# Performance work log

Hardware: AMD Instinct MI355X
Metric: run time of the kernel (lower is better)

The kernel has to match this reference:

```python
import jax, jax.numpy as jnp
import numpy as np

N, E, T = 10000, 50000, 80000   # nodes, edges, triplets
D, H, C, CF = 16, 128, 64, 64   # n_orb, hidden_dim, conv_dim, coeffs_dim


def l2norm(v):
    # matches torch F.normalize(dim=-1): x / max(||x||_2, 1e-12)
    return v / jnp.maximum(jnp.linalg.norm(v, axis=-1, keepdims=True), 1e-12)


def setup_inputs() -> dict:
    key = jax.random.key(0)
    ks = jax.random.split(key, 16)

    def w(k, i, o):
        return jax.random.normal(k, (i, o), jnp.float32) / np.sqrt(i).astype(np.float32)

    return {
        "x": jax.random.normal(ks[0], (N, H), jnp.float32),
        "cji": jax.random.normal(ks[1], (E, D, CF), jnp.float32),
        "robs": jax.random.normal(ks[2], (E, D), jnp.float32),
        "shbs": jax.random.normal(ks[3], (T, D), jnp.float32),
        "idx_i": jax.random.randint(ks[4], (E,), 0, N),
        "idx_j": jax.random.randint(ks[5], (E,), 0, N),
        "tri_idx_k": jax.random.randint(ks[6], (T,), 0, N),
        "edge_idx_kj": jax.random.randint(ks[7], (T,), 0, E),
        "edge_idx_ji": jax.random.randint(ks[8], (T,), 0, E),
        "W_nb": w(ks[9], H, 2 * C), "b_nb": jnp.zeros((2 * C,), jnp.float32),
        "W_c1": w(ks[10], CF, C),
        "W_c2": w(ks[11], C, 2 * C),
        "W_t3": w(ks[12], C, C), "b_t3": jnp.zeros((C,), jnp.float32),
        "W_n1": w(ks[13], 2 * C, C), "b_n1": jnp.zeros((C,), jnp.float32),
        "W_n2": w(ks[14], C, C), "b_n2": jnp.zeros((C,), jnp.float32),
        "W_na": w(ks[15], C, H),
    }


def reference(x, cji, robs, shbs, idx_i, idx_j, tri_idx_k, edge_idx_kj,
              edge_idx_ji, W_nb, b_nb, W_c1, W_c2, W_t3, b_t3, W_n1, b_n1,
              W_n2, b_n2, W_na):
    silu = jax.nn.silu
    # node_before_lin + chunk
    h = x @ W_nb + b_nb                       # [N, 2C]
    xq, xk = jnp.split(h, 2, axis=-1)         # each [N, C]
    # coeffs_before_lin: act -> Dense -> act -> Dense (no biases)
    c = silu(silu(cji) @ W_c1) @ W_c2         # [E, D, 2C]
    cji2, ckj = jnp.split(c, 2, axis=-1)      # each [E, D, C]
    # triplet gathers
    ckj_g = l2norm(ckj[edge_idx_kj])          # [T, D, C]
    tbo = l2norm(jnp.einsum('td,tdh->th', shbs * robs[edge_idx_kj], ckj_g))  # [T, C]
    tbw = tbo * jax.nn.sigmoid(xk[tri_idx_k])  # [T, C]
    # scatter triplets -> edges (dim_size = robs.size(0) = E)
    agg = jax.ops.segment_sum(tbw, edge_idx_ji, num_segments=E)  # [E, C]
    tbw2 = silu(agg) @ W_t3 + b_t3            # three_lin, [E, C]
    cji3 = l2norm(cji2 * (1.0 + tbw2[:, None, :]))  # cji + cji*w, normalized
    lcao = l2norm(jnp.einsum('ed,edh->eh', robs, cji3))  # [E, C]
    # node message: node_lin on concatenated endpoint features
    m = jnp.concatenate([xq[idx_i], xq[idx_j]], axis=-1)  # [E, 2C]
    m = silu(silu(m) @ W_n1 + b_n1) @ W_n2 + b_n2          # [E, C]
    out = x + jax.ops.segment_sum(lcao * m, idx_i, num_segments=N) @ W_na
    return out
```

## Files before the change

### kernel.cpp

```cpp
#include <hip/hip_runtime.h>
#include <hip/hip_bf16.h>

#define NN 10000
#define EE 50000
#define TT 80000
#define DD 16
#define HH 128
#define CC 64

typedef __hip_bfloat16 bf16;
typedef __attribute__((ext_vector_type(8))) short bf16x8;
typedef __attribute__((ext_vector_type(4))) short bf16x4;
typedef __attribute__((ext_vector_type(4))) float f32x4;

__device__ __forceinline__ float silu_f(float x) {
  return x * __builtin_amdgcn_rcpf(1.f + __expf(-x));
}
__device__ __forceinline__ float sigm_f(float x) {
  return __builtin_amdgcn_rcpf(1.f + __expf(-x));
}

__device__ __forceinline__ short f2bs(float x) {
  __hip_bfloat16 h = __float2bfloat16(x);
  short s;
  __builtin_memcpy(&s, &h, 2);
  return s;
}

__device__ __forceinline__ float rnorm_f(float ss) {
  return __builtin_amdgcn_rcpf(fmaxf(__builtin_amdgcn_sqrtf(ss), 1e-12f));
}

__device__ __forceinline__ void bf2x(unsigned u, float& lo, float& hi) {
  lo = __uint_as_float(u << 16);
  hi = __uint_as_float(u & 0xffff0000u);
}

#define ZERO_U4 960000

__global__ __launch_bounds__(128) void k_node(
    const float* __restrict__ x, const float* __restrict__ W_nb,
    const float* __restrict__ b_nb, float* __restrict__ sxq,
    float* __restrict__ sigxk, uint4* __restrict__ zero_p) {
  __shared__ __align__(16) float xs[8][HH];
  const int t = threadIdx.x;
  const int base = blockIdx.x * 8;
#pragma unroll
  for (int i = 0; i < 8; ++i) xs[i][t] = x[(size_t)(base + i) * HH + t];
  for (int i = blockIdx.x * 128 + t; i < ZERO_U4; i += (NN / 8) * 128)
    zero_p[i] = (uint4){0u, 0u, 0u, 0u};
  __syncthreads();
  float acc[8];
  const float bb = b_nb[t];
#pragma unroll
  for (int i = 0; i < 8; ++i) acc[i] = bb;
  for (int k = 0; k < HH; k += 4) {
    const float w0 = W_nb[(k + 0) * HH + t];
    const float w1 = W_nb[(k + 1) * HH + t];
    const float w2 = W_nb[(k + 2) * HH + t];
    const float w3 = W_nb[(k + 3) * HH + t];
#pragma unroll
    for (int i = 0; i < 8; ++i) {
      const float4 xv = *(const float4*)(&xs[i][k]);
      acc[i] = fmaf(xv.x, w0, acc[i]);
      acc[i] = fmaf(xv.y, w1, acc[i]);
      acc[i] = fmaf(xv.z, w2, acc[i]);
      acc[i] = fmaf(xv.w, w3, acc[i]);
    }
  }
  if (t < CC) {
#pragma unroll
    for (int i = 0; i < 8; ++i)
      sxq[(size_t)(base + i) * CC + t] = silu_f(acc[i]);
  } else {
#pragma unroll
    for (int i = 0; i < 8; ++i)
      sigxk[(size_t)(base + i) * CC + (t - CC)] = sigm_f(acc[i]);
  }
}

#define K2_BLOCKS 2048
#define K2_TILES 50000
__global__ __launch_bounds__(256, 2) void k_coeffs(
    const float* __restrict__ cji, const float* __restrict__ W_c1,
    const float* __restrict__ W_c2, bf16* __restrict__ cji2,
    bf16* __restrict__ ckjn) {
  const int tid = threadIdx.x;
  const int w = tid >> 6, l = tid & 63;
  const int lr = l & 15, lg = l >> 4;

  bf16x4 bw1[4][4];
  bf16x4 bw2[4][8];
#pragma unroll
  for (int rt = 0; rt < 4; ++rt)
#pragma unroll
    for (int kt = 0; kt < 4; ++kt) {
      bf16x4 t;
#pragma unroll
      for (int b = 0; b < 4; ++b)
        t[b] = f2bs(W_c1[(kt * 16 + lg * 4 + b) * 64 + rt * 16 + lr]);
      bw1[rt][kt] = t;
    }
#pragma unroll
  for (int kt = 0; kt < 4; ++kt)
#pragma unroll
    for (int ct = 0; ct < 8; ++ct) {
      bf16x4 t;
#pragma unroll
      for (int b = 0; b < 4; ++b)
        t[b] = f2bs(W_c2[(kt * 16 + lg * 4 + b) * 128 + ct * 16 + lr]);
      bw2[kt][ct] = t;
    }

  const int nwave = K2_BLOCKS * 4;
  const int t0 = blockIdx.x * 4 + w;
  if (t0 >= K2_TILES) return;
  const int lane_off = lr * 64 + lg * 4;

  float4 rA[4], rB[4];
#pragma unroll
  for (int kt = 0; kt < 4; ++kt)
    rA[kt] = *(const float4*)(cji + (size_t)t0 * 1024 + lane_off + kt * 16);
  if (t0 + nwave < K2_TILES)
#pragma unroll
    for (int kt = 0; kt < 4; ++kt)
      rB[kt] = *(const float4*)(cji + (size_t)(t0 + nwave) * 1024 + lane_off + kt * 16);

  auto process = [&](int tile, float4 (&r)[4], int pref_tile) {
    bf16x4 sB[4];
#pragma unroll
    for (int kt = 0; kt < 4; ++kt) {
      bf16x4 t;
      t[0] = f2bs(silu_f(r[kt].x));
      t[1] = f2bs(silu_f(r[kt].y));
      t[2] = f2bs(silu_f(r[kt].z));
      t[3] = f2bs(silu_f(r[kt].w));
      sB[kt] = t;
    }
    if (pref_tile < K2_TILES) {
#pragma unroll
      for (int kt = 0; kt < 4; ++kt)
        r[kt] = *(const float4*)(cji + (size_t)pref_tile * 1024 + lane_off + kt * 16);
    }

    f32x4 acc1[4];
#pragma unroll
    for (int rt = 0; rt < 4; ++rt) acc1[rt] = (f32x4){0.f, 0.f, 0.f, 0.f};
#pragma unroll
    for (int rt = 0; rt < 4; ++rt)
#pragma unroll
      for (int kt = 0; kt < 4; ++kt)
        acc1[rt] = __builtin_amdgcn_mfma_f32_16x16x16bf16_1k(bw1[rt][kt], sB[kt], acc1[rt], 0, 0, 0);

    bf16x4 tf[4];
#pragma unroll
    for (int kt = 0; kt < 4; ++kt) {
      bf16x4 t;
#pragma unroll
      for (int b = 0; b < 4; ++b) t[b] = f2bs(silu_f(acc1[kt][b]));
      tf[kt] = t;
    }

    {
      f32x4 acc[4];
#pragma unroll
      for (int ct = 0; ct < 4; ++ct) acc[ct] = (f32x4){0.f, 0.f, 0.f, 0.f};
#pragma unroll
      for (int ct = 0; ct < 4; ++ct)
#pragma unroll
        for (int kt = 0; kt < 4; ++kt)
          acc[ct] = __builtin_amdgcn_mfma_f32_16x16x16bf16_1k(tf[kt], bw2[kt][ct], acc[ct], 0, 0, 0);
      union { short h[16]; uint4 u[2]; } pa;
#pragma unroll
      for (int ct = 0; ct < 4; ++ct)
#pragma unroll
        for (int j = 0; j < 4; ++j) pa.h[ct * 4 + j] = f2bs(acc[ct][j]);
      uint4* d0 = (uint4*)(cji2 + (size_t)tile * 1024 + l * 16);
      d0[0] = pa.u[0];
      d0[1] = pa.u[1];
    }

    {
      f32x4 acc[4];
#pragma unroll
      for (int ct = 0; ct < 4; ++ct) acc[ct] = (f32x4){0.f, 0.f, 0.f, 0.f};
#pragma unroll
      for (int ct = 0; ct < 4; ++ct)
#pragma unroll
        for (int kt = 0; kt < 4; ++kt)
          acc[ct] = __builtin_amdgcn_mfma_f32_16x16x16bf16_1k(tf[kt], bw2[kt][4 + ct], acc[ct], 0, 0, 0);
      float rn[4];
#pragma unroll
      for (int j = 0; j < 4; ++j) {
        float ss = acc[0][j] * acc[0][j];
        ss = fmaf(acc[1][j], acc[1][j], ss);
        ss = fmaf(acc[2][j], acc[2][j], ss);
        ss = fmaf(acc[3][j], acc[3][j], ss);
#pragma unroll
        for (int m = 1; m < 16; m <<= 1) ss += __shfl_xor(ss, m, 64);
        rn[j] = rnorm_f(ss);
      }
      union { short h[16]; uint4 u[2]; } pb;
#pragma unroll
      for (int ct = 0; ct < 4; ++ct)
#pragma unroll
        for (int j = 0; j < 4; ++j) pb.h[ct * 4 + j] = f2bs(acc[ct][j] * rn[j]);
      uint4* d1 = (uint4*)(ckjn + (size_t)tile * 1024 + l * 16);
      d1[0] = pb.u[0];
      d1[1] = pb.u[1];
    }
  };

  for (int tile = t0; tile < K2_TILES; tile += 2 * nwave) {
    process(tile, rA, tile + 2 * nwave);
    if (tile + nwave < K2_TILES)
      process(tile + nwave, rB, tile + 3 * nwave);
  }
}

#define K3_WAVES 20000
__global__ __launch_bounds__(256) void k_triplet(
    const bf16* __restrict__ ckjn, const float* __restrict__ shbs,
    const float* __restrict__ robs, const float* __restrict__ sigxk,
    const int* __restrict__ tri_idx_k, const int* __restrict__ edge_idx_kj,
    const int* __restrict__ edge_idx_ji, float* __restrict__ agg) {
  const int wid = (blockIdx.x * 256 + threadIdx.x) >> 6;
  const int l = threadIdx.x & 63;
  if (wid >= K3_WAVES) return;
  const int lq = l >> 4;
  const int t0 = wid * 4;

  int kj[4], kn[4], ji[4];
#pragma unroll
  for (int i = 0; i < 4; ++i) {
    kj[i] = edge_idx_kj[t0 + i];
    kn[i] = tri_idx_k[t0 + i];
    ji[i] = edge_idx_ji[t0 + i];
  }
  float4 sh[4], rb[4];
  uint4 u0[4], u1[4];
  float sx[4];
#pragma unroll
  for (int i = 0; i < 4; ++i) {
    sh[i] = *(const float4*)(shbs + (size_t)(t0 + i) * DD + lq * 4);
    rb[i] = *(const float4*)(robs + (size_t)kj[i] * DD + lq * 4);
    const uint4* b = (const uint4*)(ckjn + (size_t)kj[i] * 1024 + l * 16);
    u0[i] = b[0];
    u1[i] = b[1];
    sx[i] = sigxk[(size_t)kn[i] * CC + l];
  }

  float acc[4][4];
#pragma unroll
  for (int i = 0; i < 4; ++i) {
    const float w0 = sh[i].x * rb[i].x, w1 = sh[i].y * rb[i].y,
                w2 = sh[i].z * rb[i].z, w3 = sh[i].w * rb[i].w;
    float x0, x1, x2, x3;
    bf2x(u0[i].x, x0, x1); bf2x(u0[i].y, x2, x3);
    acc[i][0] = fmaf(w3, x3, fmaf(w2, x2, fmaf(w1, x1, w0 * x0)));
    bf2x(u0[i].z, x0, x1); bf2x(u0[i].w, x2, x3);
    acc[i][1] = fmaf(w3, x3, fmaf(w2, x2, fmaf(w1, x1, w0 * x0)));
    bf2x(u1[i].x, x0, x1); bf2x(u1[i].y, x2, x3);
    acc[i][2] = fmaf(w3, x3, fmaf(w2, x2, fmaf(w1, x1, w0 * x0)));
    bf2x(u1[i].z, x0, x1); bf2x(u1[i].w, x2, x3);
    acc[i][3] = fmaf(w3, x3, fmaf(w2, x2, fmaf(w1, x1, w0 * x0)));
  }
#pragma unroll
  for (int m = 16; m < 64; m <<= 1)
#pragma unroll
    for (int i = 0; i < 4; ++i)
#pragma unroll
      for (int q = 0; q < 4; ++q) acc[i][q] += __shfl_xor(acc[i][q], m, 64);

  float sel[4], ss[4];
#pragma unroll
  for (int i = 0; i < 4; ++i) {
    sel[i] = (lq == 0) ? acc[i][0] : (lq == 1) ? acc[i][1]
             : (lq == 2) ? acc[i][2] : acc[i][3];
    ss[i] = sel[i] * sel[i];
  }
#pragma unroll
  for (int m = 1; m < 64; m <<= 1)
#pragma unroll
    for (int i = 0; i < 4; ++i) ss[i] += __shfl_xor(ss[i], m, 64);
#pragma unroll
  for (int i = 0; i < 4; ++i) {
    const float tbw = sel[i] * rnorm_f(ss[i]) * sx[i];
    atomicAdd(&agg[(size_t)ji[i] * CC + l], tbw);
  }
}

#define K4A_TILES 3125
#define K4A_BLOCKS 256
__global__ __launch_bounds__(256, 2) void k_edge_a(
    const float* __restrict__ agg, const float* __restrict__ sxq,
    const int* __restrict__ idx_i, const int* __restrict__ idx_j,
    const float* __restrict__ W_t3, const float* __restrict__ b_t3,
    const float* __restrict__ W_n1, const float* __restrict__ b_n1,
    const float* __restrict__ W_n2, const float* __restrict__ b_n2,
    float* __restrict__ onew_buf, float* __restrict__ m_buf) {
  __shared__ __align__(16) float fbuf[4][16 * 68];
  __shared__ __align__(16) short sbuf[4][16 * 72];
  const int tid = threadIdx.x;
  const int w = tid >> 6, l = tid & 63;
  const int lr = l & 15, lg = l >> 4;
  float* fb = fbuf[w];
  short* sb = sbuf[w];

  bf16x8 bt3[2][4], bn1[4][4], bn2[2][4];
#pragma unroll
  for (int kt = 0; kt < 2; ++kt)
#pragma unroll
    for (int nt = 0; nt < 4; ++nt) {
      bf16x8 t;
#pragma unroll
      for (int b = 0; b < 8; ++b)
        t[b] = f2bs(W_t3[(kt * 32 + lg * 8 + b) * 64 + nt * 16 + lr]);
      bt3[kt][nt] = t;
    }
#pragma unroll
  for (int kt = 0; kt < 4; ++kt)
#pragma unroll
    for (int nt = 0; nt < 4; ++nt) {
      bf16x8 t;
#pragma unroll
      for (int b = 0; b < 8; ++b)
        t[b] = f2bs(W_n1[(kt * 32 + lg * 8 + b) * 64 + nt * 16 + lr]);
      bn1[kt][nt] = t;
    }
#pragma unroll
  for (int kt = 0; kt < 2; ++kt)
#pragma unroll
    for (int nt = 0; nt < 4; ++nt) {
      bf16x8 t;
#pragma unroll
      for (int b = 0; b < 8; ++b)
        t[b] = f2bs(W_n2[(kt * 32 + lg * 8 + b) * 64 + nt * 16 + lr]);
      bn2[kt][nt] = t;
    }
  float bt3c[4], bn1c[4], bn2c[4];
#pragma unroll
  for (int nt = 0; nt < 4; ++nt) {
    bt3c[nt] = b_t3[nt * 16 + lr];
    bn1c[nt] = b_n1[nt * 16 + lr];
    bn2c[nt] = b_n2[nt * 16 + lr];
  }

  for (int tile = blockIdx.x * 4 + w; tile < K4A_TILES; tile += K4A_BLOCKS * 4) {
    const int e = tile * 16 + lr;
    const int vi = idx_i[e], vj = idx_j[e];

    bf16x8 aagg[2];
#pragma unroll
    for (int kt = 0; kt < 2; ++kt) {
      const float4 u = *(const float4*)(agg + (size_t)e * 64 + kt * 32 + lg * 8);
      const float4 v = *(const float4*)(agg + (size_t)e * 64 + kt * 32 + lg * 8 + 4);
      bf16x8 t;
      t[0] = f2bs(silu_f(u.x)); t[1] = f2bs(silu_f(u.y));
      t[2] = f2bs(silu_f(u.z)); t[3] = f2bs(silu_f(u.w));
      t[4] = f2bs(silu_f(v.x)); t[5] = f2bs(silu_f(v.y));
      t[6] = f2bs(silu_f(v.z)); t[7] = f2bs(silu_f(v.w));
      aagg[kt] = t;
    }
    f32x4 acc[4];
#pragma unroll
    for (int nt = 0; nt < 4; ++nt) acc[nt] = (f32x4){0.f, 0.f, 0.f, 0.f};
#pragma unroll
    for (int nt = 0; nt < 4; ++nt) {
      acc[nt] = __builtin_amdgcn_mfma_f32_16x16x32_bf16(aagg[0], bt3[0][nt], acc[nt], 0, 0, 0);
      acc[nt] = __builtin_amdgcn_mfma_f32_16x16x32_bf16(aagg[1], bt3[1][nt], acc[nt], 0, 0, 0);
    }
#pragma unroll
    for (int nt = 0; nt < 4; ++nt)
#pragma unroll
      for (int j = 0; j < 4; ++j)
        fb[(lg * 4 + j) * 68 + nt * 16 + lr] = 1.f + bt3c[nt] + acc[nt][j];
    {
      const int row = l >> 2, cs = (l & 3) * 16;
      float* dst = onew_buf + (size_t)(tile * 16 + row) * 64 + cs;
#pragma unroll
      for (int q = 0; q < 4; ++q)
        *(float4*)(dst + q * 4) = *(const float4*)(fb + row * 68 + cs + q * 4);
    }

    bf16x8 am[4];
#pragma unroll
    for (int kt = 0; kt < 4; ++kt) {
      const float* src = (kt < 2) ? (sxq + (size_t)vi * 64 + kt * 32)
                                  : (sxq + (size_t)vj * 64 + (kt - 2) * 32);
      const float4 u = *(const float4*)(src + lg * 8);
      const float4 v = *(const float4*)(src + lg * 8 + 4);
      bf16x8 t;
      t[0] = f2bs(u.x); t[1] = f2bs(u.y); t[2] = f2bs(u.z); t[3] = f2bs(u.w);
      t[4] = f2bs(v.x); t[5] = f2bs(v.y); t[6] = f2bs(v.z); t[7] = f2bs(v.w);
      am[kt] = t;
    }
    f32x4 acc1[4];
#pragma unroll
    for (int nt = 0; nt < 4; ++nt) acc1[nt] = (f32x4){0.f, 0.f, 0.f, 0.f};
#pragma unroll
    for (int nt = 0; nt < 4; ++nt)
#pragma unroll
      for (int kt = 0; kt < 4; ++kt)
        acc1[nt] = __builtin_amdgcn_mfma_f32_16x16x32_bf16(am[kt], bn1[kt][nt], acc1[nt], 0, 0, 0);

#pragma unroll
    for (int nt = 0; nt < 4; ++nt)
#pragma unroll
      for (int j = 0; j < 4; ++j)
        sb[(lg * 4 + j) * 72 + nt * 16 + lr] = f2bs(silu_f(acc1[nt][j] + bn1c[nt]));
    const bf16x8 a20 = *(const bf16x8*)(sb + lr * 72 + lg * 8);
    const bf16x8 a21 = *(const bf16x8*)(sb + lr * 72 + 32 + lg * 8);

    f32x4 acc2[4];
#pragma unroll
    for (int nt = 0; nt < 4; ++nt) acc2[nt] = (f32x4){0.f, 0.f, 0.f, 0.f};
#pragma unroll
    for (int nt = 0; nt < 4; ++nt) {
      acc2[nt] = __builtin_amdgcn_mfma_f32_16x16x32_bf16(a20, bn2[0][nt], acc2[nt], 0, 0, 0);
      acc2[nt] = __builtin_amdgcn_mfma_f32_16x16x32_bf16(a21, bn2[1][nt], acc2[nt], 0, 0, 0);
    }
#pragma unroll
    for (int nt = 0; nt < 4; ++nt)
#pragma unroll
      for (int j = 0; j < 4; ++j)
        fb[(lg * 4 + j) * 68 + nt * 16 + lr] = acc2[nt][j] + bn2c[nt];
    {
      const int row = l >> 2, cs = (l & 3) * 16;
      float* dst = m_buf + (size_t)(tile * 16 + row) * 64 + cs;
#pragma unroll
      for (int q = 0; q < 4; ++q)
        *(float4*)(dst + q * 4) = *(const float4*)(fb + row * 68 + cs + q * 4);
    }
  }
}

#define K4B_WAVES 25000
__global__ __launch_bounds__(256) void k_edge_b(
    const bf16* __restrict__ cji2, const float* __restrict__ robs,
    const float* __restrict__ onew_buf, const float* __restrict__ m_buf,
    const int* __restrict__ idx_i, float* __restrict__ lacc) {
  const int wid = (blockIdx.x * 256 + threadIdx.x) >> 6;
  const int l = threadIdx.x & 63;
  if (wid >= K4B_WAVES) return;
  const int lq = l >> 4, lr = l & 15;
  const int e0 = wid * 2;

  uint4 u0[2], u1[2];
  float4 rb[2];
  float ow[2][4], mm[2];
  int vi[2];
#pragma unroll
  for (int i = 0; i < 2; ++i) {
    const uint4* base = (const uint4*)(cji2 + (size_t)(e0 + i) * 1024 + l * 16);
    u0[i] = base[0];
    u1[i] = base[1];
    const float* ob = onew_buf + (size_t)(e0 + i) * 64 + lr;
    ow[i][0] = ob[0]; ow[i][1] = ob[16]; ow[i][2] = ob[32]; ow[i][3] = ob[48];
    rb[i] = *(const float4*)(robs + (size_t)(e0 + i) * DD + lq * 4);
    mm[i] = m_buf[(size_t)(e0 + i) * 64 + l];
    vi[i] = idx_i[e0 + i];
  }

  float v[2][16];
#pragma unroll
  for (int i = 0; i < 2; ++i) {
    bf2x(u0[i].x, v[i][0], v[i][1]);   bf2x(u0[i].y, v[i][2], v[i][3]);
    bf2x(u0[i].z, v[i][4], v[i][5]);   bf2x(u0[i].w, v[i][6], v[i][7]);
    bf2x(u1[i].x, v[i][8], v[i][9]);   bf2x(u1[i].y, v[i][10], v[i][11]);
    bf2x(u1[i].z, v[i][12], v[i][13]); bf2x(u1[i].w, v[i][14], v[i][15]);
#pragma unroll
    for (int j = 0; j < 4; ++j) {
      v[i][j] *= ow[i][0];
      v[i][4 + j] *= ow[i][1];
      v[i][8 + j] *= ow[i][2];
      v[i][12 + j] *= ow[i][3];
    }
  }
  float sq[2][4];
#pragma unroll
  for (int i = 0; i < 2; ++i)
#pragma unroll
    for (int j = 0; j < 4; ++j)
      sq[i][j] = fmaf(v[i][j], v[i][j],
                 fmaf(v[i][4 + j], v[i][4 + j],
                 fmaf(v[i][8 + j], v[i][8 + j], v[i][12 + j] * v[i][12 + j])));
#pragma unroll
  for (int m = 1; m < 16; m <<= 1)
#pragma unroll
    for (int i = 0; i < 2; ++i)
#pragma unroll
      for (int j = 0; j < 4; ++j) sq[i][j] += __shfl_xor(sq[i][j], m, 64);

  float lcq[2][4];
#pragma unroll
  for (int i = 0; i < 2; ++i) {
    const float t0 = rb[i].x * rnorm_f(sq[i][0]),
                t1 = rb[i].y * rnorm_f(sq[i][1]),
                t2 = rb[i].z * rnorm_f(sq[i][2]),
                t3 = rb[i].w * rnorm_f(sq[i][3]);
#pragma unroll
    for (int q = 0; q < 4; ++q)
      lcq[i][q] = fmaf(t0, v[i][q * 4 + 0],
                  fmaf(t1, v[i][q * 4 + 1],
                  fmaf(t2, v[i][q * 4 + 2], t3 * v[i][q * 4 + 3])));
  }
#pragma unroll
  for (int m = 16; m < 64; m <<= 1)
#pragma unroll
    for (int i = 0; i < 2; ++i)
#pragma unroll
      for (int q = 0; q < 4; ++q) lcq[i][q] += __shfl_xor(lcq[i][q], m, 64);

  float sel[2], ss[2];
#pragma unroll
  for (int i = 0; i < 2; ++i) {
    sel[i] = (lq == 0) ? lcq[i][0] : (lq == 1) ? lcq[i][1]
             : (lq == 2) ? lcq[i][2] : lcq[i][3];
    ss[i] = sel[i] * sel[i];
  }
#pragma unroll
  for (int m = 1; m < 64; m <<= 1)
#pragma unroll
    for (int i = 0; i < 2; ++i) ss[i] += __shfl_xor(ss[i], m, 64);
#pragma unroll
  for (int i = 0; i < 2; ++i) {
    const float lcao = sel[i] * rnorm_f(ss[i]);
    atomicAdd(&lacc[(size_t)vi[i] * CC + l], lcao * mm[i]);
  }
}

__global__ __launch_bounds__(128) void k_out(
    const float* __restrict__ x, const float* __restrict__ lacc,
    const float* __restrict__ W_na, float* __restrict__ out) {
  __shared__ __align__(16) float ls[8][CC];
  const int t = threadIdx.x;
  const int base = blockIdx.x * 8;
  for (int idx = t; idx < 8 * CC; idx += 128)
    ls[idx >> 6][idx & 63] = lacc[(size_t)(base + (idx >> 6)) * CC + (idx & 63)];
  __syncthreads();
  float acc[8];
#pragma unroll
  for (int i = 0; i < 8; ++i) acc[i] = x[(size_t)(base + i) * HH + t];
  for (int k = 0; k < CC; k += 4) {
    const float w0 = W_na[(k + 0) * HH + t];
    const float w1 = W_na[(k + 1) * HH + t];
    const float w2 = W_na[(k + 2) * HH + t];
    const float w3 = W_na[(k + 3) * HH + t];
#pragma unroll
    for (int i = 0; i < 8; ++i) {
      const float4 lv = *(const float4*)(&ls[i][k]);
      acc[i] = fmaf(lv.x, w0, acc[i]);
      acc[i] = fmaf(lv.y, w1, acc[i]);
      acc[i] = fmaf(lv.z, w2, acc[i]);
      acc[i] = fmaf(lv.w, w3, acc[i]);
    }
  }
#pragma unroll
  for (int i = 0; i < 8; ++i) out[(size_t)(base + i) * HH + t] = acc[i];
}

extern "C" void kernel_launch(void* const* d_in, const int* in_sizes, int n_in,
                              void* d_out, int out_size, void* d_ws,
                              size_t ws_size, hipStream_t stream) {
  const float* x = (const float*)d_in[0];
  const float* cji = (const float*)d_in[1];
  const float* robs = (const float*)d_in[2];
  const float* shbs = (const float*)d_in[3];
  const int* idx_i = (const int*)d_in[4];
  const int* idx_j = (const int*)d_in[5];
  const int* tri_idx_k = (const int*)d_in[6];
  const int* edge_idx_kj = (const int*)d_in[7];
  const int* edge_idx_ji = (const int*)d_in[8];
  const float* W_nb = (const float*)d_in[9];
  const float* b_nb = (const float*)d_in[10];
  const float* W_c1 = (const float*)d_in[11];
  const float* W_c2 = (const float*)d_in[12];
  const float* W_t3 = (const float*)d_in[13];
  const float* b_t3 = (const float*)d_in[14];
  const float* W_n1 = (const float*)d_in[15];
  const float* b_n1 = (const float*)d_in[16];
  const float* W_n2 = (const float*)d_in[17];
  const float* b_n2 = (const float*)d_in[18];
  const float* W_na = (const float*)d_in[19];
  float* out = (float*)d_out;

  char* ws = (char*)d_ws;
  const size_t NC4 = (size_t)NN * CC * 4;
  const size_t EDC2 = (size_t)EE * DD * CC * 2;
  const size_t EC4 = (size_t)EE * CC * 4;
  float* sxq = (float*)(ws);
  float* sigxk = (float*)(ws + NC4);
  bf16* cji2 = (bf16*)(ws + 2 * NC4);
  bf16* ckjn = (bf16*)(ws + 2 * NC4 + EDC2);
  float* agg = (float*)(ws + 2 * NC4 + 2 * EDC2);
  float* lacc = (float*)(ws + 2 * NC4 + 2 * EDC2 + EC4);
  float* onew_buf = (float*)(ws + 2 * NC4 + EDC2);
  float* m_buf = (float*)(ws + 2 * NC4 + EDC2 + EC4);

  k_node<<<NN / 8, 128, 0, stream>>>(x, W_nb, b_nb, sxq, sigxk, (uint4*)agg);
  k_coeffs<<<K2_BLOCKS, 256, 0, stream>>>(cji, W_c1, W_c2, cji2, ckjn);
  k_triplet<<<(K3_WAVES + 3) / 4, 256, 0, stream>>>(ckjn, shbs, robs, sigxk,
                                                    tri_idx_k, edge_idx_kj,
                                                    edge_idx_ji, agg);
  k_edge_a<<<K4A_BLOCKS, 256, 0, stream>>>(
      agg, sxq, idx_i, idx_j, W_t3, b_t3, W_n1, b_n1, W_n2, b_n2, onew_buf,
      m_buf);
  k_edge_b<<<(K4B_WAVES + 3) / 4, 256, 0, stream>>>(cji2, robs, onew_buf,
                                                    m_buf, idx_i, lacc);
  k_out<<<NN / 8, 128, 0, stream>>>(x, lacc, W_na, out);
}
```

Measured before the change: 194.0 us.

## Stage cji tiles through LDS via async global_load_lds double buffering

The coeffs kernel previously loaded each cji tile straight into registers with strided float4 loads and a two-tile register prefetch. It now issues direct global-to-LDS loads (global_load_lds) into a per-wave double buffer with an XOR swizzle, waits on vmcnt, and reads the tile back from LDS in the MFMA operand layout. The aim is fully coalesced contiguous global reads and lower register pressure while keeping the next tile's load in flight. In exchange it uses 32KB of LDS per block, which can limit occupancy, and depends on hand-written waitcnt ordering being correct.

```diff
diff --git a/kernel.cpp b/kernel.cpp
--- a/kernel.cpp
+++ b/kernel.cpp
@@ -85,6 +85,7 @@
     const float* __restrict__ cji, const float* __restrict__ W_c1,
     const float* __restrict__ W_c2, bf16* __restrict__ cji2,
     bf16* __restrict__ ckjn) {
+  __shared__ __align__(16) float abuf[4][2][1024];
   const int tid = threadIdx.x;
   const int w = tid >> 6, l = tid & 63;
   const int lr = l & 15, lg = l >> 4;
@@ -112,35 +113,56 @@
       bw2[kt][ct] = t;
     }
 
+  int stg[4], rdi[4];
+#pragma unroll
+  for (int q = 0; q < 4; ++q) {
+    const int o = q * 1024 + l * 16;
+    stg[q] = o ^ (((o >> 8) & 7) << 4);
+  }
+#pragma unroll
+  for (int kt = 0; kt < 4; ++kt) {
+    const int g = lr * 256 + kt * 64 + lg * 16;
+    rdi[kt] = (g ^ ((lr & 7) << 4)) >> 2;
+  }
+
   const int nwave = K2_BLOCKS * 4;
-  const int t0 = blockIdx.x * 4 + w;
-  if (t0 >= K2_TILES) return;
-  const int lane_off = lr * 64 + lg * 4;
-
-  float4 rA[4], rB[4];
-#pragma unroll
-  for (int kt = 0; kt < 4; ++kt)
-    rA[kt] = *(const float4*)(cji + (size_t)t0 * 1024 + lane_off + kt * 16);
-  if (t0 + nwave < K2_TILES)
-#pragma unroll
-    for (int kt = 0; kt < 4; ++kt)
-      rB[kt] = *(const float4*)(cji + (size_t)(t0 + nwave) * 1024 + lane_off + kt * 16);
-
-  auto process = [&](int tile, float4 (&r)[4], int pref_tile) {
+  int tile = blockIdx.x * 4 + w;
+  if (tile >= K2_TILES) return;
+
+  {
+    const char* tb = (const char*)(cji + (size_t)tile * 1024);
+#pragma unroll
+    for (int q = 0; q < 4; ++q)
+      __builtin_amdgcn_global_load_lds((const uint4*)(tb + stg[q]),
+                                       &abuf[w][0][q * 256], 16, 0, 0);
+  }
+  int cur = 0;
+
+  for (; tile < K2_TILES; tile += nwave, cur ^= 1) {
+    const int next = tile + nwave;
+    if (next < K2_TILES) {
+      const char* tb = (const char*)(cji + (size_t)next * 1024);
+#pragma unroll
+      for (int q = 0; q < 4; ++q)
+        __builtin_amdgcn_global_load_lds((const uint4*)(tb + stg[q]),
+                                         &abuf[w][cur ^ 1][q * 256], 16, 0, 0);
+      asm volatile("s_waitcnt vmcnt(4)" ::: "memory");
+    } else {
+      asm volatile("s_waitcnt vmcnt(0)" ::: "memory");
+    }
+    __builtin_amdgcn_sched_barrier(0);
+    const float* ab = abuf[w][cur];
+
     bf16x4 sB[4];
 #pragma unroll
     for (int kt = 0; kt < 4; ++kt) {
+      const float4 r = *(const float4*)(ab + rdi[kt]);
       bf16x4 t;
-      t[0] = f2bs(silu_f(r[kt].x));
-      t[1] = f2bs(silu_f(r[kt].y));
-      t[2] = f2bs(silu_f(r[kt].z));
-      t[3] = f2bs(silu_f(r[kt].w));
+      t[0] = f2bs(silu_f(r.x));
+      t[1] = f2bs(silu_f(r.y));
+      t[2] = f2bs(silu_f(r.z));
+      t[3] = f2bs(silu_f(r.w));
       sB[kt] = t;
-    }
-    if (pref_tile < K2_TILES) {
-#pragma unroll
-      for (int kt = 0; kt < 4; ++kt)
-        r[kt] = *(const float4*)(cji + (size_t)pref_tile * 1024 + lane_off + kt * 16);
     }
 
     f32x4 acc1[4];
@@ -209,12 +231,6 @@
       d1[0] = pb.u[0];
       d1[1] = pb.u[1];
     }
-  };
-
-  for (int tile = t0; tile < K2_TILES; tile += 2 * nwave) {
-    process(tile, rA, tile + 2 * nwave);
-    if (tile + nwave < K2_TILES)
-      process(tile + nwave, rB, tile + 3 * nwave);
   }
 }
 
```

Measured after the change: 196.7 us. About the same (+1.3%).

## Stage coeff MLP weights in LDS and raise k_coeffs occupancy

Applied to the files above, without the earlier changes.

Moves the bf16-converted W_c1/W_c2 MFMA fragments from per-lane registers into shared memory, loaded once per block, and reads them from LDS inside the MFMA loops. Launch bounds go from 2 to 4 blocks per CU to raise occupancy. The manual two-tile register prefetch of cji is dropped in favour of a simple grid-stride loop. The aim is to free VGPRs and hide the latency of the large cji stream through more resident waves, at the cost of extra LDS reads per tile and no explicit software prefetch.

```diff
diff --git a/kernel.cpp b/kernel.cpp
--- a/kernel.cpp
+++ b/kernel.cpp
@@ -81,82 +81,71 @@
 
 #define K2_BLOCKS 2048
 #define K2_TILES 50000
-__global__ __launch_bounds__(256, 2) void k_coeffs(
+__global__ __launch_bounds__(256, 4) void k_coeffs(
     const float* __restrict__ cji, const float* __restrict__ W_c1,
     const float* __restrict__ W_c2, bf16* __restrict__ cji2,
     bf16* __restrict__ ckjn) {
+  __shared__ __align__(16) short lw1[16 * 64 * 4];
+  __shared__ __align__(16) short lw2[32 * 64 * 4];
   const int tid = threadIdx.x;
   const int w = tid >> 6, l = tid & 63;
   const int lr = l & 15, lg = l >> 4;
 
-  bf16x4 bw1[4][4];
-  bf16x4 bw2[4][8];
-#pragma unroll
-  for (int rt = 0; rt < 4; ++rt)
+  for (int fl = tid; fl < 16 * 64; fl += 256) {
+    const int f = fl >> 6, ll = fl & 63;
+    const int rt = f >> 2, kt = f & 3;
+    const int llr = ll & 15, llg = ll >> 4;
+    union { short h[4]; uint2 u; } t;
+#pragma unroll
+    for (int b = 0; b < 4; ++b)
+      t.h[b] = f2bs(W_c1[(kt * 16 + llg * 4 + b) * 64 + rt * 16 + llr]);
+    *(uint2*)(lw1 + fl * 4) = t.u;
+  }
+  for (int fl = tid; fl < 32 * 64; fl += 256) {
+    const int f = fl >> 6, ll = fl & 63;
+    const int kt = f >> 3, ct = f & 7;
+    const int llr = ll & 15, llg = ll >> 4;
+    union { short h[4]; uint2 u; } t;
+#pragma unroll
+    for (int b = 0; b < 4; ++b)
+      t.h[b] = f2bs(W_c2[(kt * 16 + llg * 4 + b) * 128 + ct * 16 + llr]);
+    *(uint2*)(lw2 + fl * 4) = t.u;
+  }
+  __syncthreads();
+
+  const int nwave = K2_BLOCKS * 4;
+  const int lane_off = lr * 64 + lg * 4;
+
+  for (int tile = blockIdx.x * 4 + w; tile < K2_TILES; tile += nwave) {
+    const float* Ab = cji + (size_t)tile * 1024 + lane_off;
+    bf16x4 sB[4];
+#pragma unroll
+    for (int kt = 0; kt < 4; ++kt) {
+      const float4 r = *(const float4*)(Ab + kt * 16);
+      bf16x4 t;
+      t[0] = f2bs(silu_f(r.x));
+      t[1] = f2bs(silu_f(r.y));
+      t[2] = f2bs(silu_f(r.z));
+      t[3] = f2bs(silu_f(r.w));
+      sB[kt] = t;
+    }
+
+    f32x4 acc1[4];
+#pragma unroll
+    for (int rt = 0; rt < 4; ++rt) acc1[rt] = (f32x4){0.f, 0.f, 0.f, 0.f};
+#pragma unroll
+    for (int rt = 0; rt < 4; ++rt)
+#pragma unroll
+      for (int kt = 0; kt < 4; ++kt) {
+        const bf16x4 wv = *(const bf16x4*)(lw1 + ((rt * 4 + kt) * 64 + l) * 4);
+        acc1[rt] = __builtin_amdgcn_mfma_f32_16x16x16bf16_1k(wv, sB[kt], acc1[rt], 0, 0, 0);
+      }
+
+    bf16x4 tf[4];
 #pragma unroll
     for (int kt = 0; kt < 4; ++kt) {
       bf16x4 t;
 #pragma unroll
-      for (int b = 0; b < 4; ++b)
-        t[b] = f2bs(W_c1[(kt * 16 + lg * 4 + b) * 64 + rt * 16 + lr]);
-      bw1[rt][kt] = t;
-    }
-#pragma unroll
-  for (int kt = 0; kt < 4; ++kt)
-#pragma unroll
-    for (int ct = 0; ct < 8; ++ct) {
-      bf16x4 t;
-#pragma unroll
-      for (int b = 0; b < 4; ++b)
-        t[b] = f2bs(W_c2[(kt * 16 + lg * 4 + b) * 128 + ct * 16 + lr]);
-      bw2[kt][ct] = t;
-    }
-
-  const int nwave = K2_BLOCKS * 4;
-  const int t0 = blockIdx.x * 4 + w;
-  if (t0 >= K2_TILES) return;
-  const int lane_off = lr * 64 + lg * 4;
-
-  float4 rA[4], rB[4];
-#pragma unroll
-  for (int kt = 0; kt < 4; ++kt)
-    rA[kt] = *(const float4*)(cji + (size_t)t0 * 1024 + lane_off + kt * 16);
-  if (t0 + nwave < K2_TILES)
-#pragma unroll
-    for (int kt = 0; kt < 4; ++kt)
-      rB[kt] = *(const float4*)(cji + (size_t)(t0 + nwave) * 1024 + lane_off + kt * 16);
-
-  auto process = [&](int tile, float4 (&r)[4], int pref_tile) {
-    bf16x4 sB[4];
-#pragma unroll
-    for (int kt = 0; kt < 4; ++kt) {
-      bf16x4 t;
-      t[0] = f2bs(silu_f(r[kt].x));
-      t[1] = f2bs(silu_f(r[kt].y));
-      t[2] = f2bs(silu_f(r[kt].z));
-      t[3] = f2bs(silu_f(r[kt].w));
-      sB[kt] = t;
-    }
-    if (pref_tile < K2_TILES) {
-#pragma unroll
-      for (int kt = 0; kt < 4; ++kt)
-        r[kt] = *(const float4*)(cji + (size_t)pref_tile * 1024 + lane_off + kt * 16);
-    }
-
-    f32x4 acc1[4];
-#pragma unroll
-    for (int rt = 0; rt < 4; ++rt) acc1[rt] = (f32x4){0.f, 0.f, 0.f, 0.f};
-#pragma unroll
-    for (int rt = 0; rt < 4; ++rt)
-#pragma unroll
-      for (int kt = 0; kt < 4; ++kt)
-        acc1[rt] = __builtin_amdgcn_mfma_f32_16x16x16bf16_1k(bw1[rt][kt], sB[kt], acc1[rt], 0, 0, 0);
-
-    bf16x4 tf[4];
-#pragma unroll
-    for (int kt = 0; kt < 4; ++kt) {
-      bf16x4 t;
-#pragma unroll
       for (int b = 0; b < 4; ++b) t[b] = f2bs(silu_f(acc1[kt][b]));
       tf[kt] = t;
     }
@@ -168,8 +157,10 @@
 #pragma unroll
       for (int ct = 0; ct < 4; ++ct)
 #pragma unroll
-        for (int kt = 0; kt < 4; ++kt)
-          acc[ct] = __builtin_amdgcn_mfma_f32_16x16x16bf16_1k(tf[kt], bw2[kt][ct], acc[ct], 0, 0, 0);
+        for (int kt = 0; kt < 4; ++kt) {
+          const bf16x4 wv = *(const bf16x4*)(lw2 + ((kt * 8 + ct) * 64 + l) * 4);
+          acc[ct] = __builtin_amdgcn_mfma_f32_16x16x16bf16_1k(tf[kt], wv, acc[ct], 0, 0, 0);
+        }
       union { short h[16]; uint4 u[2]; } pa;
 #pragma unroll
       for (int ct = 0; ct < 4; ++ct)
@@ -187,8 +178,10 @@
 #pragma unroll
       for (int ct = 0; ct < 4; ++ct)
 #pragma unroll
-        for (int kt = 0; kt < 4; ++kt)
-          acc[ct] = __builtin_amdgcn_mfma_f32_16x16x16bf16_1k(tf[kt], bw2[kt][4 + ct], acc[ct], 0, 0, 0);
+        for (int kt = 0; kt < 4; ++kt) {
+          const bf16x4 wv = *(const bf16x4*)(lw2 + ((kt * 8 + 4 + ct) * 64 + l) * 4);
+          acc[ct] = __builtin_amdgcn_mfma_f32_16x16x16bf16_1k(tf[kt], wv, acc[ct], 0, 0, 0);
+        }
       float rn[4];
 #pragma unroll
       for (int j = 0; j < 4; ++j) {
@@ -209,12 +202,6 @@
       d1[0] = pb.u[0];
       d1[1] = pb.u[1];
     }
-  };
-
-  for (int tile = t0; tile < K2_TILES; tile += 2 * nwave) {
-    process(tile, rA, tile + 2 * nwave);
-    if (tile + nwave < K2_TILES)
-      process(tile + nwave, rB, tile + 3 * nwave);
   }
 }
 
```

New measurement: 224.1 us. 15.5% more time.
